# Optimization experiments

Measured on AMD Instinct MI355X. Metric: run time of the kernel, lower is better.

Reference implementation:

```python
import jax, jax.numpy as jnp
import numpy as np

N_NODES = 100000
N_EDGES = 1600000
IN_DIM = 256
OUT_DIM = 32


def setup_inputs() -> dict:
    key = jax.random.key(0)
    k1, k2, k3, k4, k5 = jax.random.split(key, 5)
    x = jax.random.normal(k1, (N_NODES, IN_DIM), dtype=jnp.float32)
    src = jax.random.randint(k2, (N_EDGES,), 0, N_NODES, dtype=jnp.int32)
    dst = jax.random.randint(k3, (N_EDGES,), 0, N_NODES, dtype=jnp.int32)
    # GraphConv parameters (DGL: weight [in, out], bias [out])
    W = jax.random.normal(k4, (IN_DIM, OUT_DIM), dtype=jnp.float32) / np.sqrt(IN_DIM)
    b = jnp.zeros((OUT_DIM,), dtype=jnp.float32)
    return {"x": x, "src": src, "dst": dst, "W": W, "b": b}


def reference(x, src, dst, W, b):
    # DGL GraphConv, norm='both', allow_zero_in_degree=True:
    #   out = D_in^{-1/2} A D_out^{-1/2} X W + b  (degrees clamped to min 1)
    ones = jnp.ones(src.shape[0], dtype=x.dtype)
    deg_out = jax.ops.segment_sum(ones, src, num_segments=N_NODES)
    deg_in = jax.ops.segment_sum(ones, dst, num_segments=N_NODES)
    norm_src = jnp.clip(deg_out, 1.0, None) ** -0.5  # [N]
    norm_dst = jnp.clip(deg_in, 1.0, None) ** -0.5   # [N]
    # in_dim > out_dim: project first (smaller messages), then aggregate
    h = (x * norm_src[:, None]) @ W                  # [N, out]
    msgs = h[src]                                    # [E, out] gather
    agg = jax.ops.segment_sum(msgs, dst, num_segments=N_NODES)  # [N, out]
    return agg * norm_dst[:, None] + b
```

## Files before the change

kernel.cpp:

```cpp
#include <hip/hip_runtime.h>

#define N_NODES 100000
#define N_EDGES 1600000
#define IN_DIM 256
#define OUT_DIM 32

#define SB_SHIFT 7
#define NSB ((N_NODES + 127) >> 7)
#define SBCAP 2368
#define EBLK 2048
#define NB1 ((N_EDGES + EBLK - 1) / EBLK)
#define NGB ((N_NODES + 255) / 256)

typedef __attribute__((ext_vector_type(8))) short short8;
typedef __attribute__((ext_vector_type(16))) float f32x16;

#define WT_STRIDE 264

__device__ inline unsigned short f2bf(float f) {
    unsigned u = __float_as_uint(f);
    unsigned r = u + 0x7FFF + ((u >> 16) & 1);
    return (unsigned short)(r >> 16);
}
__device__ inline float bf2f(unsigned short us) {
    return __uint_as_float((unsigned)us << 16);
}

__global__ __launch_bounds__(512) void k_mega(const int* __restrict__ src,
                                              const int* __restrict__ dst,
                                              unsigned long long* __restrict__ qcnt,
                                              unsigned* __restrict__ gsb,
                                              unsigned char* __restrict__ gss,
                                              const float* __restrict__ x,
                                              const float* __restrict__ W,
                                              unsigned short* __restrict__ h2) {
    __shared__ __align__(16) int smemI[6 * NSB + 2 * EBLK];
    const int tid = threadIdx.x;
    const int bid = blockIdx.x;
    const int g = bid / 3;
    const int rem = bid - g * 3;

    if (rem == 0) {
        unsigned short* WT = (unsigned short*)smemI;
        #pragma unroll
        for (int i = 0; i < 16; ++i) {
            int idx = tid + i * 512;
            WT[(idx & 31) * WT_STRIDE + (idx >> 5)] = f2bf(W[idx]);
        }
        __syncthreads();

        const int wv = tid >> 6;
        const int lane = tid & 63;
        const int col = lane & 31;
        const int hi = lane >> 5;

        const int row0 = g * 256 + wv * 32;
        int grow = row0 + col;
        int growc = grow < N_NODES ? grow : N_NODES - 1;
        const float4* xrow = reinterpret_cast<const float4*>(x + (size_t)growc * IN_DIM);

        f32x16 acc = {0.f,0.f,0.f,0.f,0.f,0.f,0.f,0.f,
                      0.f,0.f,0.f,0.f,0.f,0.f,0.f,0.f};

        #pragma unroll 4
        for (int t = 0; t < 16; ++t) {
            int k4 = t * 4 + hi * 2;
            float4 p0 = xrow[k4];
            float4 p1 = xrow[k4 + 1];
            short8 a;
            a[0] = (short)f2bf(p0.x); a[1] = (short)f2bf(p0.y);
            a[2] = (short)f2bf(p0.z); a[3] = (short)f2bf(p0.w);
            a[4] = (short)f2bf(p1.x); a[5] = (short)f2bf(p1.y);
            a[6] = (short)f2bf(p1.z); a[7] = (short)f2bf(p1.w);
            short8 bfr = *reinterpret_cast<const short8*>(
                &WT[col * WT_STRIDE + t * 16 + hi * 8]);
            acc = __builtin_amdgcn_mfma_f32_32x32x16_bf16(a, bfr, acc, 0, 0, 0);
        }

        #pragma unroll
        for (int r = 0; r < 16; ++r) {
            int rowi = (r & 3) + 8 * (r >> 2) + 4 * hi;
            int go = row0 + rowi;
            if (go < N_NODES)
                h2[(size_t)go * OUT_DIM + col] = f2bf(acc[r]);
        }
    } else {
        const int pb = 2 * g + rem - 1;
        int* hist    = smemI;
        int* bbase   = smemI + NSB;
        int* cur     = smemI + 2 * NSB;
        int* hist_s  = smemI + 3 * NSB;
        int* bbase_s = smemI + 4 * NSB;
        int* cur_s   = smemI + 5 * NSB;
        int* es      = smemI + 6 * NSB;
        int* ed      = smemI + 6 * NSB + EBLK;

        const int e0 = pb * EBLK;
        const int n = min(EBLK, N_EDGES - e0);

        for (int i = tid; i < NSB; i += 512) {
            hist[i] = 0; cur[i] = 0; hist_s[i] = 0; cur_s[i] = 0;
        }
        __syncthreads();

        for (int i = tid; i < n; i += 512) {
            int s = src[e0 + i];
            int d = dst[e0 + i];
            es[i] = s; ed[i] = d;
            atomicAdd(&hist[d >> SB_SHIFT], 1);
            atomicAdd(&hist_s[s >> SB_SHIFT], 1);
        }
        __syncthreads();

        for (int i = tid; i < NSB; i += 512) {
            unsigned long long pack =
                ((unsigned long long)(unsigned)hist_s[i] << 32) | (unsigned)hist[i];
            unsigned long long old = atomicAdd(&qcnt[i], pack);
            bbase[i]   = (int)(old & 0xFFFFFFFFull);
            bbase_s[i] = (int)(old >> 32);
        }
        __syncthreads();

        for (int i = tid; i < n; i += 512) {
            int d = ed[i];
            int s = es[i];
            int r = d >> SB_SHIFT;
            int lp = atomicAdd(&cur[r], 1);
            int pos = bbase[r] + lp;
            if (pos < SBCAP)
                gsb[(size_t)r * SBCAP + pos] = ((unsigned)(d & 127) << 17) | (unsigned)s;
            int rs = s >> SB_SHIFT;
            int lp2 = atomicAdd(&cur_s[rs], 1);
            int pos2 = bbase_s[rs] + lp2;
            if (pos2 < SBCAP)
                gss[(size_t)rs * SBCAP + pos2] = (unsigned char)(s & 127);
        }
    }
}

__global__ __launch_bounds__(256) void k_deg2(const int* __restrict__ qcnt2,
                                              const unsigned char* __restrict__ gss,
                                              float* __restrict__ nrmtab) {
    __shared__ int hist[128];
    const int r = blockIdx.x;
    const int tid = threadIdx.x;
    if (tid < 128) hist[tid] = 0;
    __syncthreads();
    int cnt = qcnt2[2 * r + 1];
    if (cnt > SBCAP) cnt = SBCAP;
    const unsigned char* bp = gss + (size_t)r * SBCAP;
    for (int i = tid; i < cnt; i += 256)
        atomicAdd(&hist[bp[i]], 1);
    __syncthreads();
    if (tid < 128) {
        int nn = (r << SB_SHIFT) + tid;
        if (nn < N_NODES) {
            int dg = hist[tid];
            nrmtab[nn] = rsqrtf((float)(dg > 1 ? dg : 1));
        }
    }
}

__global__ __launch_bounds__(512) void k_combo2(const int* __restrict__ qcnt2,
                                                const unsigned* __restrict__ gsb,
                                                const unsigned short* __restrict__ h2,
                                                const float* __restrict__ nrmtab,
                                                const float* __restrict__ bias,
                                                float* __restrict__ out) {
    __shared__ unsigned pstage[SBCAP];
    __shared__ int esl[SBCAP];
    __shared__ int hist[128];
    __shared__ int pref[128];
    __shared__ int cur[128];

    const int r = blockIdx.x;
    const int tid = threadIdx.x;

    if (tid < 128) { hist[tid] = 0; cur[tid] = 0; }
    int cnt = qcnt2[2 * r];
    if (cnt > SBCAP) cnt = SBCAP;
    const unsigned* bp = gsb + (size_t)r * SBCAP;
    __syncthreads();

    for (int i = tid; i < cnt; i += 512) {
        unsigned pay = bp[i];
        pstage[i] = pay;
        atomicAdd(&hist[pay >> 17], 1);
    }
    __syncthreads();

    int v = 0;
    if (tid < 128) { v = hist[tid]; pref[tid] = v; }
    __syncthreads();
    #pragma unroll
    for (int off = 1; off < 128; off <<= 1) {
        int t = (tid < 128 && tid >= off) ? pref[tid - off] : 0;
        __syncthreads();
        if (tid < 128) pref[tid] += t;
        __syncthreads();
    }
    if (tid < 128) pref[tid] -= v;
    __syncthreads();

    for (int i = tid; i < cnt; i += 512) {
        unsigned pay = pstage[i];
        int l = (int)(pay >> 17);
        int lp = atomicAdd(&cur[l], 1);
        esl[pref[l] + lp] = (int)(pay & 0x1FFFF);
    }
    __syncthreads();

    const int q = tid & 7;
    const int nl = tid >> 3;
    const float4 bb = reinterpret_cast<const float4*>(bias)[q];
    #pragma unroll
    for (int sweep = 0; sweep < 2; ++sweep) {
        int l = sweep * 64 + nl;
        int st = pref[l];
        int deg = hist[l];
        float4 acc = make_float4(0.f, 0.f, 0.f, 0.f);
        int j = 0;
        for (; j + 4 <= deg; j += 4) {
            int s0 = esl[st + j + 0];
            int s1 = esl[st + j + 1];
            int s2 = esl[st + j + 2];
            int s3 = esl[st + j + 3];
            float w0 = nrmtab[s0];
            float w1 = nrmtab[s1];
            float w2 = nrmtab[s2];
            float w3 = nrmtab[s3];
            ushort4 a0 = *reinterpret_cast<const ushort4*>(&h2[(size_t)s0 * OUT_DIM + q * 4]);
            ushort4 a1 = *reinterpret_cast<const ushort4*>(&h2[(size_t)s1 * OUT_DIM + q * 4]);
            ushort4 a2 = *reinterpret_cast<const ushort4*>(&h2[(size_t)s2 * OUT_DIM + q * 4]);
            ushort4 a3 = *reinterpret_cast<const ushort4*>(&h2[(size_t)s3 * OUT_DIM + q * 4]);
            acc.x += bf2f(a0.x) * w0 + bf2f(a1.x) * w1 + bf2f(a2.x) * w2 + bf2f(a3.x) * w3;
            acc.y += bf2f(a0.y) * w0 + bf2f(a1.y) * w1 + bf2f(a2.y) * w2 + bf2f(a3.y) * w3;
            acc.z += bf2f(a0.z) * w0 + bf2f(a1.z) * w1 + bf2f(a2.z) * w2 + bf2f(a3.z) * w3;
            acc.w += bf2f(a0.w) * w0 + bf2f(a1.w) * w1 + bf2f(a2.w) * w2 + bf2f(a3.w) * w3;
        }
        for (; j < deg; ++j) {
            int s = esl[st + j];
            float w = nrmtab[s];
            ushort4 a = *reinterpret_cast<const ushort4*>(&h2[(size_t)s * OUT_DIM + q * 4]);
            acc.x += bf2f(a.x) * w; acc.y += bf2f(a.y) * w;
            acc.z += bf2f(a.z) * w; acc.w += bf2f(a.w) * w;
        }
        int node = (r << SB_SHIFT) + l;
        if (node < N_NODES) {
            float nrm = rsqrtf((float)(deg > 1 ? deg : 1));
            float4 o = make_float4(acc.x * nrm + bb.x, acc.y * nrm + bb.y,
                                   acc.z * nrm + bb.z, acc.w * nrm + bb.w);
            reinterpret_cast<float4*>(out)[(size_t)node * 8 + q] = o;
        }
    }
}

extern "C" void kernel_launch(void* const* d_in, const int* in_sizes, int n_in,
                              void* d_out, int out_size, void* d_ws, size_t ws_size,
                              hipStream_t stream) {
    const float* x   = (const float*)d_in[0];
    const int*   src = (const int*)d_in[1];
    const int*   dst = (const int*)d_in[2];
    const float* W   = (const float*)d_in[3];
    const float* b   = (const float*)d_in[4];
    float* out = (float*)d_out;

    float* nrmtab = (float*)d_ws;
    unsigned long long* qcnt = (unsigned long long*)(nrmtab + N_NODES);
    int* qcnt2 = (int*)qcnt;
    unsigned short* h2 = (unsigned short*)((char*)d_ws + 406272);
    unsigned* gsb = (unsigned*)(h2 + (size_t)N_NODES * OUT_DIM);
    unsigned char* gss = (unsigned char*)(gsb + (size_t)NSB * SBCAP);

    hipMemsetAsync(qcnt, 0, NSB * sizeof(unsigned long long), stream);

    k_mega<<<NB1 + NGB, 512, 0, stream>>>(src, dst, qcnt, gsb, gss, x, W, h2);

    k_deg2<<<NSB, 256, 0, stream>>>(qcnt2, gss, nrmtab);

    k_combo2<<<NSB, 512, 0, stream>>>(qcnt2, gsb, h2, nrmtab, b, out);
}
```

Before: 88.37 us.

## Coarsen edge buckets to 1024-node chunks and build a global CSR before gathering

Edges are bucketed by 1024-node chunks instead of 128-node chunks, so the first pass needs far fewer shared-memory counters and global atomics per block. A new split kernel with 1024 threads per chunk builds a global CSR (row_ptr, deg_in, esrc) and the out-degree norms in a single launch. The gather kernel then reads the CSR from global memory rather than re-sorting each bucket in LDS. In exchange, the split phase has only 196 large blocks, which limits parallelism, and the CSR makes an extra global write and read round trip.

```diff
diff --git a/kernel.cpp b/kernel.cpp
--- a/kernel.cpp
+++ b/kernel.cpp
@@ -5,9 +5,9 @@
 #define IN_DIM 256
 #define OUT_DIM 32
 
-#define SB_SHIFT 7
-#define NSB ((N_NODES + 127) >> 7)
-#define SBCAP 2368
+#define CSH 10
+#define NSBC 98
+#define SBC 17152
 #define EBLK 2048
 #define NB1 ((N_EDGES + EBLK - 1) / EBLK)
 #define NGB ((N_NODES + 255) / 256)
@@ -30,11 +30,11 @@
                                               const int* __restrict__ dst,
                                               unsigned long long* __restrict__ qcnt,
                                               unsigned* __restrict__ gsb,
-                                              unsigned char* __restrict__ gss,
+                                              unsigned short* __restrict__ gss,
                                               const float* __restrict__ x,
                                               const float* __restrict__ W,
                                               unsigned short* __restrict__ h2) {
-    __shared__ __align__(16) int smemI[6 * NSB + 2 * EBLK];
+    __shared__ __align__(16) int smemI[6 * NSBC + 2 * EBLK];
     const int tid = threadIdx.x;
     const int bid = blockIdx.x;
     const int g = bid / 3;
@@ -86,20 +86,20 @@
         }
     } else {
         const int pb = 2 * g + rem - 1;
-        int* hist    = smemI;
-        int* bbase   = smemI + NSB;
-        int* cur     = smemI + 2 * NSB;
-        int* hist_s  = smemI + 3 * NSB;
-        int* bbase_s = smemI + 4 * NSB;
-        int* cur_s   = smemI + 5 * NSB;
-        int* es      = smemI + 6 * NSB;
-        int* ed      = smemI + 6 * NSB + EBLK;
+        int* histD = smemI;
+        int* bbD   = smemI + NSBC;
+        int* curD  = smemI + 2 * NSBC;
+        int* histS = smemI + 3 * NSBC;
+        int* bbS   = smemI + 4 * NSBC;
+        int* curS  = smemI + 5 * NSBC;
+        int* es    = smemI + 6 * NSBC;
+        int* ed    = smemI + 6 * NSBC + EBLK;
 
         const int e0 = pb * EBLK;
         const int n = min(EBLK, N_EDGES - e0);
 
-        for (int i = tid; i < NSB; i += 512) {
-            hist[i] = 0; cur[i] = 0; hist_s[i] = 0; cur_s[i] = 0;
+        if (tid < NSBC) {
+            histD[tid] = 0; curD[tid] = 0; histS[tid] = 0; curS[tid] = 0;
         }
         __syncthreads();
 
@@ -107,124 +107,133 @@
             int s = src[e0 + i];
             int d = dst[e0 + i];
             es[i] = s; ed[i] = d;
-            atomicAdd(&hist[d >> SB_SHIFT], 1);
-            atomicAdd(&hist_s[s >> SB_SHIFT], 1);
-        }
-        __syncthreads();
-
-        for (int i = tid; i < NSB; i += 512) {
+            atomicAdd(&histD[d >> CSH], 1);
+            atomicAdd(&histS[s >> CSH], 1);
+        }
+        __syncthreads();
+
+        if (tid < NSBC) {
             unsigned long long pack =
-                ((unsigned long long)(unsigned)hist_s[i] << 32) | (unsigned)hist[i];
-            unsigned long long old = atomicAdd(&qcnt[i], pack);
-            bbase[i]   = (int)(old & 0xFFFFFFFFull);
-            bbase_s[i] = (int)(old >> 32);
+                ((unsigned long long)(unsigned)histS[tid] << 32) | (unsigned)histD[tid];
+            unsigned long long old = atomicAdd(&qcnt[tid], pack);
+            bbD[tid] = (int)(old & 0xFFFFFFFFull);
+            bbS[tid] = (int)(old >> 32);
         }
         __syncthreads();
 
         for (int i = tid; i < n; i += 512) {
             int d = ed[i];
             int s = es[i];
-            int r = d >> SB_SHIFT;
-            int lp = atomicAdd(&cur[r], 1);
-            int pos = bbase[r] + lp;
-            if (pos < SBCAP)
-                gsb[(size_t)r * SBCAP + pos] = ((unsigned)(d & 127) << 17) | (unsigned)s;
-            int rs = s >> SB_SHIFT;
-            int lp2 = atomicAdd(&cur_s[rs], 1);
-            int pos2 = bbase_s[rs] + lp2;
-            if (pos2 < SBCAP)
-                gss[(size_t)rs * SBCAP + pos2] = (unsigned char)(s & 127);
+            int r = d >> CSH;
+            int lp = atomicAdd(&curD[r], 1);
+            int pos = bbD[r] + lp;
+            if (pos < SBC)
+                gsb[(size_t)r * SBC + pos] = ((unsigned)(d & 1023) << 17) | (unsigned)s;
+            int rs = s >> CSH;
+            int lp2 = atomicAdd(&curS[rs], 1);
+            int pos2 = bbS[rs] + lp2;
+            if (pos2 < SBC)
+                gss[(size_t)rs * SBC + pos2] = (unsigned short)(s & 1023);
         }
     }
 }
 
-__global__ __launch_bounds__(256) void k_deg2(const int* __restrict__ qcnt2,
-                                              const unsigned char* __restrict__ gss,
-                                              float* __restrict__ nrmtab) {
-    __shared__ int hist[128];
-    const int r = blockIdx.x;
+__global__ __launch_bounds__(1024) void k_split(const int* __restrict__ qcnt2,
+                                                const unsigned* __restrict__ gsb,
+                                                const unsigned short* __restrict__ gss,
+                                                int* __restrict__ esrc,
+                                                int* __restrict__ row_ptr,
+                                                int* __restrict__ deg_in,
+                                                float* __restrict__ nrmtab) {
+    __shared__ int hist[1024];
+    __shared__ int pref[1024];
+    __shared__ int cur[1024];
     const int tid = threadIdx.x;
-    if (tid < 128) hist[tid] = 0;
-    __syncthreads();
-    int cnt = qcnt2[2 * r + 1];
-    if (cnt > SBCAP) cnt = SBCAP;
-    const unsigned char* bp = gss + (size_t)r * SBCAP;
-    for (int i = tid; i < cnt; i += 256)
-        atomicAdd(&hist[bp[i]], 1);
-    __syncthreads();
-    if (tid < 128) {
-        int nn = (r << SB_SHIFT) + tid;
-        if (nn < N_NODES) {
+    const int bid = blockIdx.x;
+
+    if (bid < NSBC) {
+        const int r = bid;
+        hist[tid] = 0; cur[tid] = 0;
+        __syncthreads();
+
+        int cnt = qcnt2[2 * r];
+        if (cnt > SBC) cnt = SBC;
+        const unsigned* bp = gsb + (size_t)r * SBC;
+
+        for (int i = tid; i < cnt; i += 1024)
+            atomicAdd(&hist[bp[i] >> 17], 1);
+        __syncthreads();
+
+        int v = hist[tid];
+        pref[tid] = v;
+        __syncthreads();
+        #pragma unroll
+        for (int off = 1; off < 1024; off <<= 1) {
+            int t = (tid >= off) ? pref[tid - off] : 0;
+            __syncthreads();
+            pref[tid] += t;
+            __syncthreads();
+        }
+        int excl = pref[tid] - v;
+
+        const int rbase = r * SBC;
+        int n = (r << CSH) + tid;
+        if (n < N_NODES) {
+            row_ptr[n] = rbase + excl;
+            deg_in[n] = v;
+        }
+        pref[tid] = excl;
+        __syncthreads();
+
+        for (int i = tid; i < cnt; i += 1024) {
+            unsigned pay = bp[i];
+            int l = (int)(pay >> 17);
+            int lp = atomicAdd(&cur[l], 1);
+            esrc[rbase + pref[l] + lp] = (int)(pay & 0x1FFFF);
+        }
+    } else {
+        const int r = bid - NSBC;
+        hist[tid] = 0;
+        __syncthreads();
+        int cnt = qcnt2[2 * r + 1];
+        if (cnt > SBC) cnt = SBC;
+        const unsigned short* sp = gss + (size_t)r * SBC;
+        for (int i = tid; i < cnt; i += 1024)
+            atomicAdd(&hist[sp[i]], 1);
+        __syncthreads();
+        int n = (r << CSH) + tid;
+        if (n < N_NODES) {
             int dg = hist[tid];
-            nrmtab[nn] = rsqrtf((float)(dg > 1 ? dg : 1));
+            nrmtab[n] = rsqrtf((float)(dg > 1 ? dg : 1));
         }
     }
 }
 
-__global__ __launch_bounds__(512) void k_combo2(const int* __restrict__ qcnt2,
-                                                const unsigned* __restrict__ gsb,
+__global__ __launch_bounds__(512) void k_gather(const int* __restrict__ esrc,
+                                                const int* __restrict__ row_ptr,
+                                                const int* __restrict__ deg_in,
                                                 const unsigned short* __restrict__ h2,
                                                 const float* __restrict__ nrmtab,
                                                 const float* __restrict__ bias,
                                                 float* __restrict__ out) {
-    __shared__ unsigned pstage[SBCAP];
-    __shared__ int esl[SBCAP];
-    __shared__ int hist[128];
-    __shared__ int pref[128];
-    __shared__ int cur[128];
-
-    const int r = blockIdx.x;
     const int tid = threadIdx.x;
-
-    if (tid < 128) { hist[tid] = 0; cur[tid] = 0; }
-    int cnt = qcnt2[2 * r];
-    if (cnt > SBCAP) cnt = SBCAP;
-    const unsigned* bp = gsb + (size_t)r * SBCAP;
-    __syncthreads();
-
-    for (int i = tid; i < cnt; i += 512) {
-        unsigned pay = bp[i];
-        pstage[i] = pay;
-        atomicAdd(&hist[pay >> 17], 1);
-    }
-    __syncthreads();
-
-    int v = 0;
-    if (tid < 128) { v = hist[tid]; pref[tid] = v; }
-    __syncthreads();
-    #pragma unroll
-    for (int off = 1; off < 128; off <<= 1) {
-        int t = (tid < 128 && tid >= off) ? pref[tid - off] : 0;
-        __syncthreads();
-        if (tid < 128) pref[tid] += t;
-        __syncthreads();
-    }
-    if (tid < 128) pref[tid] -= v;
-    __syncthreads();
-
-    for (int i = tid; i < cnt; i += 512) {
-        unsigned pay = pstage[i];
-        int l = (int)(pay >> 17);
-        int lp = atomicAdd(&cur[l], 1);
-        esl[pref[l] + lp] = (int)(pay & 0x1FFFF);
-    }
-    __syncthreads();
-
     const int q = tid & 7;
     const int nl = tid >> 3;
     const float4 bb = reinterpret_cast<const float4*>(bias)[q];
+
     #pragma unroll
     for (int sweep = 0; sweep < 2; ++sweep) {
-        int l = sweep * 64 + nl;
-        int st = pref[l];
-        int deg = hist[l];
+        int node = blockIdx.x * 128 + sweep * 64 + nl;
+        if (node >= N_NODES) continue;
+        int st = row_ptr[node];
+        int deg = deg_in[node];
         float4 acc = make_float4(0.f, 0.f, 0.f, 0.f);
         int j = 0;
         for (; j + 4 <= deg; j += 4) {
-            int s0 = esl[st + j + 0];
-            int s1 = esl[st + j + 1];
-            int s2 = esl[st + j + 2];
-            int s3 = esl[st + j + 3];
+            int s0 = esrc[st + j + 0];
+            int s1 = esrc[st + j + 1];
+            int s2 = esrc[st + j + 2];
+            int s3 = esrc[st + j + 3];
             float w0 = nrmtab[s0];
             float w1 = nrmtab[s1];
             float w2 = nrmtab[s2];
@@ -239,19 +248,16 @@
             acc.w += bf2f(a0.w) * w0 + bf2f(a1.w) * w1 + bf2f(a2.w) * w2 + bf2f(a3.w) * w3;
         }
         for (; j < deg; ++j) {
-            int s = esl[st + j];
+            int s = esrc[st + j];
             float w = nrmtab[s];
             ushort4 a = *reinterpret_cast<const ushort4*>(&h2[(size_t)s * OUT_DIM + q * 4]);
             acc.x += bf2f(a.x) * w; acc.y += bf2f(a.y) * w;
             acc.z += bf2f(a.z) * w; acc.w += bf2f(a.w) * w;
         }
-        int node = (r << SB_SHIFT) + l;
-        if (node < N_NODES) {
-            float nrm = rsqrtf((float)(deg > 1 ? deg : 1));
-            float4 o = make_float4(acc.x * nrm + bb.x, acc.y * nrm + bb.y,
-                                   acc.z * nrm + bb.z, acc.w * nrm + bb.w);
-            reinterpret_cast<float4*>(out)[(size_t)node * 8 + q] = o;
-        }
+        float nrm = rsqrtf((float)(deg > 1 ? deg : 1));
+        float4 o = make_float4(acc.x * nrm + bb.x, acc.y * nrm + bb.y,
+                               acc.z * nrm + bb.z, acc.w * nrm + bb.w);
+        reinterpret_cast<float4*>(out)[(size_t)node * 8 + q] = o;
     }
 }
 
@@ -266,17 +272,20 @@
     float* out = (float*)d_out;
 
     float* nrmtab = (float*)d_ws;
-    unsigned long long* qcnt = (unsigned long long*)(nrmtab + N_NODES);
-    int* qcnt2 = (int*)qcnt;
-    unsigned short* h2 = (unsigned short*)((char*)d_ws + 406272);
-    unsigned* gsb = (unsigned*)(h2 + (size_t)N_NODES * OUT_DIM);
-    unsigned char* gss = (unsigned char*)(gsb + (size_t)NSB * SBCAP);
-
-    hipMemsetAsync(qcnt, 0, NSB * sizeof(unsigned long long), stream);
+    int* row_ptr  = (int*)((char*)d_ws + 400000);
+    int* deg_in   = (int*)((char*)d_ws + 800000);
+    unsigned long long* qcnt = (unsigned long long*)((char*)d_ws + 1200000);
+    int* qcnt2    = (int*)qcnt;
+    unsigned short* h2 = (unsigned short*)((char*)d_ws + 1200800);
+    unsigned* gsb = (unsigned*)((char*)d_ws + 7600800);
+    unsigned short* gss = (unsigned short*)((char*)d_ws + 14324384);
+    int* esrc     = (int*)((char*)d_ws + 17686176);
+
+    hipMemsetAsync(qcnt, 0, NSBC * sizeof(unsigned long long), stream);
 
     k_mega<<<NB1 + NGB, 512, 0, stream>>>(src, dst, qcnt, gsb, gss, x, W, h2);
 
-    k_deg2<<<NSB, 256, 0, stream>>>(qcnt2, gss, nrmtab);
-
-    k_combo2<<<NSB, 512, 0, stream>>>(qcnt2, gsb, h2, nrmtab, b, out);
-}
+    k_split<<<2 * NSBC, 1024, 0, stream>>>(qcnt2, gsb, gss, esrc, row_ptr, deg_in, nrmtab);
+
+    k_gather<<<(N_NODES + 127) / 128, 512, 0, stream>>>(esrc, row_ptr, deg_in, h2, nrmtab, b, out);
+}
```

New measurement: 104.9 us. 18.7% more time.
